# Performance work log

Measured on AMD Instinct MI355X. Metric: run time of the kernel, lower is better.

The kernel has to match this reference:

```python
import jax, jax.numpy as jnp
import numpy as np

EPS = 1e-8  # F.cosine_similarity eps
K = 2       # prompt_length


def setup_inputs() -> dict:
    key = jax.random.key(0)
    k1, k2, k3, k4 = jax.random.split(key, 4)
    B, DIM, NP, D = 32, 64, 4, 1024   # P: [batch, dim, N_p, D]; D == V (rows of stored table)
    E, VC = 768, 32000                 # stored table [V=D, E]; f_e: E -> vocab_dim=VC
    P = jax.random.normal(k1, (B, DIM, NP, D), dtype=jnp.float32)
    we_stored = jax.random.normal(k2, (D, E), dtype=jnp.float32) * 0.02
    fe_w = jax.random.normal(k3, (VC, E), dtype=jnp.float32) * 0.02
    fe_b = jax.random.normal(k4, (VC,), dtype=jnp.float32) * 0.02
    return {"P": P, "we_stored": we_stored, "fe_w": fe_w, "fe_b": fe_b}


def reference(P, we_stored, fe_w, fe_b):
    # word_embeddings = f_e(stored).t()  ->  [vocab_dim, V] == [VC, D]
    T = (we_stored @ fe_w.T + fe_b).T            # [VC, D]
    B, DIM, NP, D = P.shape
    # Cosine sim of each tiled embedding row (repeated N_p times) vs flattened P_i:
    #   dot(tiled_w, P_flat) = w . sum_j P[..., j, :]
    #   ||tiled_w|| = sqrt(N_p) * ||w||
    s = P.sum(axis=2)                                             # [B, DIM, D]
    w_norm = jnp.maximum(jnp.sqrt(jnp.float32(NP)) * jnp.linalg.norm(T, axis=1), EPS)   # [VC]
    p_norm = jnp.maximum(jnp.linalg.norm(P.reshape(B, DIM, -1), axis=-1), EPS)          # [B, DIM]
    scores = jnp.einsum('bdk,vk->bdv', s, T) / (w_norm[None, None, :] * p_norm[..., None])  # [B, DIM, VC]
    values, indices = jax.lax.top_k(scores, K)                    # [B, DIM, K]
    e_k = T[indices]                                              # [B, DIM, K, D]
    Z = jnp.concatenate([e_k, P], axis=2)                         # [B, DIM, NP+K, D]
    return Z, values
```

## Files before the change

kernel.cpp:

```cpp
#include <hip/hip_runtime.h>
#include <hip/hip_bf16.h>
#include <math.h>

#define B_    32
#define DIM_  64
#define NP_   4
#define D_    1024
#define E_    768
#define VC_   32000
#define R_    2048
#define KTOP  2
#define EPS_  1e-8f
#define NCB   250
#define NCAND 8

#define T_OFF    ((size_t)0)
#define S_OFF    (T_OFF + (size_t)VC_ * D_)
#define INVW_OFF (S_OFF + (size_t)R_ * D_)
#define INVP_OFF (INVW_OFF + VC_)
#define WSQ_OFF  (INVP_OFF + R_)
#define PV_OFF   (WSQ_OFF + VC_)
#define PI_OFF   (PV_OFF + (size_t)R_ * NCB * 2)
#define SB_OFF   (PI_OFF + (size_t)R_ * NCB * 2)
#define TB_OFF   (SB_OFF + (size_t)R_ * D_ / 2)
#define WH_OFF   (TB_OFF + (size_t)VC_ * D_ / 2)
#define WL_OFF   (WH_OFF + (size_t)D_ * E_ / 2)
#define CAND_OFF (WL_OFF + (size_t)D_ * E_ / 2)
#define TIDX_OFF (CAND_OFF + (size_t)R_ * NCAND)

#define NEG_INF (-3.4e38f)

typedef __bf16 bf16x8 __attribute__((ext_vector_type(8)));
typedef unsigned short u16x8 __attribute__((ext_vector_type(8)));
typedef float  f32x4  __attribute__((ext_vector_type(4)));

__device__ __forceinline__ unsigned short f2bf(float f) {
    unsigned u = __float_as_uint(f);
    u += 0x7fffu + ((u >> 16) & 1u);
    return (unsigned short)(u >> 16);
}

__device__ __forceinline__ void async_ld16(const void* gptr, void* lptr) {
    __builtin_amdgcn_global_load_lds(
        (const __attribute__((address_space(1))) void*)(uintptr_t)gptr,
        (__attribute__((address_space(3))) void*)(unsigned)(uintptr_t)lptr,
        16, 0, 0);
}

__device__ __forceinline__ bool better(float v, int i, float bv, int bi) {
    return (v > bv) || (v == bv && i < bi);
}

__global__ __launch_bounds__(256) void k_zero(float* __restrict__ wsq) {
    int i = blockIdx.x * 256 + threadIdx.x;
    if (i < VC_) wsq[i] = 0.f;
}

__global__ __launch_bounds__(256) void k_split_we(const float* __restrict__ x,
                                                  unsigned short* __restrict__ hi,
                                                  unsigned short* __restrict__ lo) {
    int i = (blockIdx.x * 256 + threadIdx.x) * 4;
    float4 v = *(const float4*)(x + i);
    ushort4 h, l;
    float e;
    h.x = f2bf(v.x); e = v.x - __uint_as_float((unsigned)h.x << 16); l.x = f2bf(e);
    h.y = f2bf(v.y); e = v.y - __uint_as_float((unsigned)h.y << 16); l.y = f2bf(e);
    h.z = f2bf(v.z); e = v.z - __uint_as_float((unsigned)h.z << 16); l.z = f2bf(e);
    h.w = f2bf(v.w); e = v.w - __uint_as_float((unsigned)h.w << 16); l.w = f2bf(e);
    *(ushort4*)(hi + i) = h;
    *(ushort4*)(lo + i) = l;
}

__global__ __launch_bounds__(256) void k_sum_pnorm(const float* __restrict__ P,
                                                   float* __restrict__ s,
                                                   unsigned short* __restrict__ sb,
                                                   float* __restrict__ invp) {
    int r = blockIdx.x;
    int t = threadIdx.x;
    const float* base = P + (size_t)r * NP_ * D_;
    float4 acc = make_float4(0.f, 0.f, 0.f, 0.f);
    float sq = 0.f;
#pragma unroll
    for (int np = 0; np < NP_; ++np) {
        float4 v = *(const float4*)(base + (size_t)np * D_ + t * 4);
        acc.x += v.x; acc.y += v.y; acc.z += v.z; acc.w += v.w;
        sq += v.x * v.x + v.y * v.y + v.z * v.z + v.w * v.w;
    }
    *(float4*)(s + (size_t)r * D_ + t * 4) = acc;
    ushort4 o;
    o.x = f2bf(acc.x); o.y = f2bf(acc.y); o.z = f2bf(acc.z); o.w = f2bf(acc.w);
    *(ushort4*)(sb + (size_t)r * D_ + t * 4) = o;

    __shared__ float red[256];
    red[t] = sq;
    __syncthreads();
    for (int off = 128; off > 0; off >>= 1) {
        if (t < off) red[t] += red[t + off];
        __syncthreads();
    }
    if (t == 0) invp[r] = 1.0f / fmaxf(sqrtf(red[0]), EPS_);
}

__global__ __launch_bounds__(256) void k_gemm_T_mfma(const float* __restrict__ A,
                                                     const unsigned short* __restrict__ Bh,
                                                     const unsigned short* __restrict__ Bl,
                                                     const float* __restrict__ bias,
                                                     float* __restrict__ T,
                                                     unsigned short* __restrict__ Tb,
                                                     float* __restrict__ wsq) {
    __shared__ __align__(16) float          Af[128 * 32];
    __shared__ __align__(16) unsigned short Bsh[128 * 32];
    __shared__ __align__(16) unsigned short Bsl[128 * 32];

    int tid = threadIdx.x;
    int wid = tid >> 6, lane = tid & 63;
    int quad = lane >> 4, l15 = lane & 15;
    int id  = blockIdx.x;
    int swz = (id & 7) * 250 + (id >> 3);
    int v0 = (swz >> 3) * 128;
    int d0 = (swz & 7) * 128;
    int vband = (wid & 1) * 64, nband = (wid >> 1) * 64;

    f32x4 acc[4][4];
#pragma unroll
    for (int i = 0; i < 4; ++i)
#pragma unroll
        for (int j = 0; j < 4; ++j) acc[i][j] = f32x4{0.f, 0.f, 0.f, 0.f};

    int arow = wid * 32 + (lane >> 3);
    int acol = (lane & 7) * 4;
    int brow = wid * 32 + (lane >> 2);
    int bcol = (lane & 3) * 8;

    for (int k0 = 0; k0 < E_; k0 += 32) {
#pragma unroll
        for (int j = 0; j < 4; ++j)
            async_ld16(A + (size_t)(v0 + arow + j * 8) * E_ + k0 + acol,
                       (void*)(Af + (wid * 32 + j * 8) * 32));
#pragma unroll
        for (int j = 0; j < 2; ++j) {
            async_ld16(Bh + (size_t)(d0 + brow + j * 16) * E_ + k0 + bcol,
                       (void*)(Bsh + (wid * 32 + j * 16) * 32));
            async_ld16(Bl + (size_t)(d0 + brow + j * 16) * E_ + k0 + bcol,
                       (void*)(Bsl + (wid * 32 + j * 16) * 32));
        }
        __syncthreads();

        bf16x8 bh[4], bl[4];
#pragma unroll
        for (int nt = 0; nt < 4; ++nt) {
            bh[nt] = *(const bf16x8*)(Bsh + (nband + nt * 16 + l15) * 32 + quad * 8);
            bl[nt] = *(const bf16x8*)(Bsl + (nband + nt * 16 + l15) * 32 + quad * 8);
        }
#pragma unroll
        for (int mt = 0; mt < 4; ++mt) {
            const float* ap = Af + (vband + mt * 16 + l15) * 32 + quad * 8;
            f32x4 xa = *(const f32x4*)ap;
            f32x4 xb = *(const f32x4*)(ap + 4);
            bf16x8 ah, al;
#pragma unroll
            for (int e = 0; e < 4; ++e) {
                __bf16 h0 = (__bf16)xa[e];
                __bf16 h1 = (__bf16)xb[e];
                ah[e] = h0; ah[e + 4] = h1;
                al[e]     = (__bf16)(xa[e] - (float)h0);
                al[e + 4] = (__bf16)(xb[e] - (float)h1);
            }
#pragma unroll
            for (int nt = 0; nt < 4; ++nt) {
                acc[mt][nt] = __builtin_amdgcn_mfma_f32_16x16x32_bf16(ah, bh[nt], acc[mt][nt], 0, 0, 0);
                acc[mt][nt] = __builtin_amdgcn_mfma_f32_16x16x32_bf16(al, bh[nt], acc[mt][nt], 0, 0, 0);
                acc[mt][nt] = __builtin_amdgcn_mfma_f32_16x16x32_bf16(ah, bl[nt], acc[mt][nt], 0, 0, 0);
            }
        }
        __syncthreads();
    }

    float sq[4][4] = {};
#pragma unroll
    for (int mt = 0; mt < 4; ++mt) {
        int vbase = v0 + vband + mt * 16 + quad * 4;
        float bv[4];
#pragma unroll
        for (int rg = 0; rg < 4; ++rg) bv[rg] = bias[vbase + rg];
#pragma unroll
        for (int nt = 0; nt < 4; ++nt) {
            int d = d0 + nband + nt * 16 + l15;
#pragma unroll
            for (int rg = 0; rg < 4; ++rg) {
                float val = acc[mt][nt][rg] + bv[rg];
                T[(size_t)(vbase + rg) * D_ + d] = val;
                __bf16 vb = (__bf16)val;
                Tb[(size_t)(vbase + rg) * D_ + d] = __builtin_bit_cast(unsigned short, vb);
                sq[mt][rg] += val * val;
            }
        }
    }
#pragma unroll
    for (int mt = 0; mt < 4; ++mt)
#pragma unroll
        for (int rg = 0; rg < 4; ++rg) {
            float p = sq[mt][rg];
            p += __shfl_xor(p, 1); p += __shfl_xor(p, 2);
            p += __shfl_xor(p, 4); p += __shfl_xor(p, 8);
            if (l15 == 0) atomicAdd(&wsq[v0 + vband + mt * 16 + quad * 4 + rg], p);
        }
}

__global__ __launch_bounds__(256) void k_invw(const float* __restrict__ wsq,
                                              float* __restrict__ invw) {
    int v = blockIdx.x * 256 + threadIdx.x;
    if (v < VC_) invw[v] = 1.0f / fmaxf(2.0f * sqrtf(wsq[v]), EPS_);
}

__global__ __launch_bounds__(256) void k_scores_mfma(const unsigned short* __restrict__ Tb,
                                                     const unsigned short* __restrict__ sb,
                                                     const float* __restrict__ invw,
                                                     float* __restrict__ pval,
                                                     int* __restrict__ pidx) {
    __shared__ __align__(16) unsigned short As[2][128 * 32];
    __shared__ __align__(16) unsigned short Bs[2][128 * 32];
    __shared__ float mv[2][128][2];
    __shared__ int   mi[2][128][2];

    int tid = threadIdx.x;
    int wid = tid >> 6, lane = tid & 63;
    int quad = lane >> 4, l15 = lane & 15;
    int id   = blockIdx.x;
    int swz  = (id & 7) * 500 + (id >> 3);
    int vblk = swz >> 4;
    int rblk = swz & 15;
    int v0 = vblk * 128;
    int r0 = rblk * 128;
    int vband = (wid & 1) * 64, rband = (wid >> 1) * 64;

    f32x4 acc[4][4];
#pragma unroll
    for (int i = 0; i < 4; ++i)
#pragma unroll
        for (int j = 0; j < 4; ++j) acc[i][j] = f32x4{0.f, 0.f, 0.f, 0.f};

    int r_lane = lane >> 2;
    int slot   = lane & 3;

#define STAGE_SC(buf, kk)                                                          \
    {                                                                              \
_Pragma("unroll")                                                                  \
        for (int j = 0; j < 2; ++j) {                                              \
            int rowt = wid * 32 + j * 16 + r_lane;                                 \
            int ss = (slot - (rowt >> 1)) & 3;                                     \
            async_ld16(Tb + (size_t)(v0 + rowt) * D_ + (kk) + ss * 8,              \
                       (void*)(As[buf] + (wid * 32 + j * 16) * 32));               \
            async_ld16(sb + (size_t)(r0 + rowt) * D_ + (kk) + ss * 8,              \
                       (void*)(Bs[buf] + (wid * 32 + j * 16) * 32));               \
        }                                                                          \
    }

    int cur = 0;
    STAGE_SC(0, 0);
    __syncthreads();

    for (int k0 = 0; k0 < D_; k0 += 32) {
        if (k0 + 32 < D_) STAGE_SC(cur ^ 1, k0 + 32);

        bf16x8 af[4], bfr[4];
#pragma unroll
        for (int mt = 0; mt < 4; ++mt) {
            int row = vband + mt * 16 + l15;
            int ps = (quad + (row >> 1)) & 3;
            af[mt] = *(const bf16x8*)(As[cur] + row * 32 + ps * 8);
        }
#pragma unroll
        for (int nt = 0; nt < 4; ++nt) {
            int row = rband + nt * 16 + l15;
            int ps = (quad + (row >> 1)) & 3;
            bfr[nt] = *(const bf16x8*)(Bs[cur] + row * 32 + ps * 8);
        }
#pragma unroll
        for (int mt = 0; mt < 4; ++mt)
#pragma unroll
            for (int nt = 0; nt < 4; ++nt)
                acc[mt][nt] = __builtin_amdgcn_mfma_f32_16x16x32_bf16(af[mt], bfr[nt], acc[mt][nt], 0, 0, 0);

        __syncthreads();
        cur ^= 1;
    }

    float iw[4][4];
#pragma unroll
    for (int mt = 0; mt < 4; ++mt)
#pragma unroll
        for (int rg = 0; rg < 4; ++rg)
            iw[mt][rg] = invw[v0 + vband + mt * 16 + quad * 4 + rg];

#pragma unroll
    for (int nt = 0; nt < 4; ++nt) {
        float b1 = NEG_INF, b2 = NEG_INF;
        int i1 = 0x7fffffff, i2 = 0x7fffffff;
#pragma unroll
        for (int mt = 0; mt < 4; ++mt)
#pragma unroll
            for (int rg = 0; rg < 4; ++rg) {
                float val = acc[mt][nt][rg] * iw[mt][rg];
                int v = v0 + vband + mt * 16 + quad * 4 + rg;
                if (better(val, v, b1, i1)) { b2 = b1; i2 = i1; b1 = val; i1 = v; }
                else if (better(val, v, b2, i2)) { b2 = val; i2 = v; }
            }
#pragma unroll
        for (int off = 16; off <= 32; off <<= 1) {
            float o1 = __shfl_xor(b1, off), o2 = __shfl_xor(b2, off);
            int  oi1 = __shfl_xor(i1, off), oi2 = __shfl_xor(i2, off);
            if (better(o1, oi1, b1, i1)) {
                if (better(b1, i1, o2, oi2)) { b2 = b1; i2 = i1; } else { b2 = o2; i2 = oi2; }
                b1 = o1; i1 = oi1;
            } else if (better(o1, oi1, b2, i2)) { b2 = o1; i2 = oi1; }
        }
        if (quad == 0) {
            int rl = rband + nt * 16 + l15;
            mv[wid & 1][rl][0] = b1; mi[wid & 1][rl][0] = i1;
            mv[wid & 1][rl][1] = b2; mi[wid & 1][rl][1] = i2;
        }
    }
    __syncthreads();
    if (tid < 128) {
        float b1 = mv[0][tid][0], b2 = mv[0][tid][1];
        int   i1 = mi[0][tid][0], i2 = mi[0][tid][1];
#pragma unroll
        for (int sl = 0; sl < 2; ++sl) {
            float o = mv[1][tid][sl]; int oi = mi[1][tid][sl];
            if (better(o, oi, b1, i1)) { b2 = b1; i2 = i1; b1 = o; i1 = oi; }
            else if (better(o, oi, b2, i2)) { b2 = o; i2 = oi; }
        }
        size_t off = ((size_t)(r0 + tid) * NCB + vblk) * 2;
        pval[off] = b1;     pidx[off] = i1;
        pval[off + 1] = b2; pidx[off + 1] = i2;
    }
#undef STAGE_SC
}

__global__ __launch_bounds__(256) void k_topk8(const float* __restrict__ pval,
                                               const int* __restrict__ pidx,
                                               int* __restrict__ cands) {
    int r = blockIdx.x, t = threadIdx.x;
    __shared__ float v[512];
    __shared__ int  id[512];
    for (int c = t; c < 512; c += 256) {
        if (c < NCB * 2) { v[c] = pval[(size_t)r * NCB * 2 + c]; id[c] = pidx[(size_t)r * NCB * 2 + c]; }
        else             { v[c] = NEG_INF; id[c] = 0x7fffffff; }
    }
    __syncthreads();
    if (t == 0) {
        float bv[NCAND]; int bi[NCAND];
#pragma unroll
        for (int j = 0; j < NCAND; ++j) { bv[j] = NEG_INF; bi[j] = 0x7fffffff; }
        for (int c = 0; c < NCB * 2; ++c) {
            float x = v[c]; int xi = id[c];
            if (better(x, xi, bv[NCAND - 1], bi[NCAND - 1])) {
                int j = NCAND - 1;
                while (j > 0 && better(x, xi, bv[j - 1], bi[j - 1])) {
                    bv[j] = bv[j - 1]; bi[j] = bi[j - 1]; --j;
                }
                bv[j] = x; bi[j] = xi;
            }
        }
#pragma unroll
        for (int j = 0; j < NCAND; ++j) cands[r * NCAND + j] = bi[j];
    }
}

__global__ __launch_bounds__(256) void k_rescore(const float* __restrict__ s,
                                                 const float* __restrict__ T,
                                                 const int* __restrict__ cands,
                                                 const float* __restrict__ invw,
                                                 const float* __restrict__ invp,
                                                 float* __restrict__ outv,
                                                 int* __restrict__ tidx) {
    int r = blockIdx.x, t = threadIdx.x;
    int cg = t >> 5, l32 = t & 31;
    int c = cands[r * NCAND + cg];
    const float* Trow = T + (size_t)c * D_;
    const float* srow = s + (size_t)r * D_;
    float p = 0.f;
#pragma unroll
    for (int j = 0; j < 8; ++j) {
        int e = (j * 32 + l32) * 4;
        float4 a = *(const float4*)(srow + e);
        float4 b = *(const float4*)(Trow + e);
        p += a.x * b.x + a.y * b.y + a.z * b.z + a.w * b.w;
    }
#pragma unroll
    for (int off = 16; off >= 1; off >>= 1) p += __shfl_xor(p, off);
    __shared__ float sc[NCAND];
    if (l32 == 0) sc[cg] = p;
    __syncthreads();
    if (t == 0) {
        float ip = invp[r];
        float b1 = NEG_INF, b2 = NEG_INF;
        int i1 = 0x7fffffff, i2 = 0x7fffffff;
#pragma unroll
        for (int j = 0; j < NCAND; ++j) {
            int ci = cands[r * NCAND + j];
            float val = sc[j] * invw[ci] * ip;
            if (better(val, ci, b1, i1)) { b2 = b1; i2 = i1; b1 = val; i1 = ci; }
            else if (better(val, ci, b2, i2)) { b2 = val; i2 = ci; }
        }
        outv[(size_t)r * 2 + 0] = b1;
        outv[(size_t)r * 2 + 1] = b2;
        tidx[r * 2 + 0] = i1;
        tidx[r * 2 + 1] = i2;
    }
}

__global__ __launch_bounds__(256) void k_writeZ(const float* __restrict__ P,
                                                const float* __restrict__ T,
                                                const int* __restrict__ tidx,
                                                float* __restrict__ out) {
    int blk = blockIdx.x;
    int r = blk / 6, j = blk - r * 6;
    const float* src;
    if (j < KTOP) src = T + (size_t)tidx[r * 2 + j] * D_;
    else          src = P + ((size_t)r * NP_ + (j - KTOP)) * D_;
    float4 v = *(const float4*)(src + threadIdx.x * 4);
    *(float4*)(out + ((size_t)r * 6 + j) * D_ + threadIdx.x * 4) = v;
}

extern "C" void kernel_launch(void* const* d_in, const int* in_sizes, int n_in,
                              void* d_out, int out_size, void* d_ws, size_t ws_size,
                              hipStream_t stream) {
    const float* P   = (const float*)d_in[0];
    const float* we  = (const float*)d_in[1];
    const float* few = (const float*)d_in[2];
    const float* feb = (const float*)d_in[3];
    float* out = (float*)d_out;
    float* ws  = (float*)d_ws;

    float* T    = ws + T_OFF;
    float* s    = ws + S_OFF;
    float* invw = ws + INVW_OFF;
    float* invp = ws + INVP_OFF;
    float* wsq  = ws + WSQ_OFF;
    float* pval = ws + PV_OFF;
    int*   pidx = (int*)(ws + PI_OFF);
    unsigned short* sb  = (unsigned short*)(ws + SB_OFF);
    unsigned short* Tb  = (unsigned short*)(ws + TB_OFF);
    unsigned short* weh = (unsigned short*)(ws + WH_OFF);
    unsigned short* wel = (unsigned short*)(ws + WL_OFF);
    int*   cands = (int*)(ws + CAND_OFF);
    int*   tidx  = (int*)(ws + TIDX_OFF);
    float* outv = out + (size_t)R_ * 6 * D_;

    k_zero<<<(VC_ + 255) / 256, 256, 0, stream>>>(wsq);
    k_split_we<<<(D_ * E_) / 1024, 256, 0, stream>>>(we, weh, wel);
    k_sum_pnorm<<<R_, 256, 0, stream>>>(P, s, sb, invp);
    k_gemm_T_mfma<<<2000, 256, 0, stream>>>(few, weh, wel, feb, T, Tb, wsq);
    k_invw<<<(VC_ + 255) / 256, 256, 0, stream>>>(wsq, invw);
    k_scores_mfma<<<4000, 256, 0, stream>>>(Tb, sb, invw, pval, pidx);
    k_topk8<<<R_, 256, 0, stream>>>(pval, pidx, cands);
    k_rescore<<<R_, 256, 0, stream>>>(s, T, cands, invw, invp, outv, tidx);
    k_writeZ<<<R_ * 6, 256, 0, stream>>>(P, T, tidx, out);
}
```

Baseline: 683.1 us.

## Pre-split fe_w to bf16 hi/lo and double-buffer T GEMM with swizzled LDS

A separate pass now splits fe_w into bf16 hi/lo arrays once, instead of converting fp32 A tiles inside the GEMM inner loop for every d-block. The T GEMM loads all four operands with async global-to-LDS copies into double buffers, prefetching the next k-slice while the current one is computed. It also rotates 16-byte slots per row to cut LDS bank conflicts. The cost is an extra kernel and about 98MB of extra workspace traffic, plus twice the LDS footprint, which may lower occupancy. The f2bf helper is also replaced by native bf16 casts.

```diff
diff --git a/kernel.cpp b/kernel.cpp
--- a/kernel.cpp
+++ b/kernel.cpp
@@ -27,18 +27,14 @@
 #define WL_OFF   (WH_OFF + (size_t)D_ * E_ / 2)
 #define CAND_OFF (WL_OFF + (size_t)D_ * E_ / 2)
 #define TIDX_OFF (CAND_OFF + (size_t)R_ * NCAND)
+#define AH_OFF   (TIDX_OFF + (size_t)R_ * 2)
+#define AL_OFF   (AH_OFF + (size_t)VC_ * E_ / 2)
 
 #define NEG_INF (-3.4e38f)
 
 typedef __bf16 bf16x8 __attribute__((ext_vector_type(8)));
 typedef unsigned short u16x8 __attribute__((ext_vector_type(8)));
 typedef float  f32x4  __attribute__((ext_vector_type(4)));
-
-__device__ __forceinline__ unsigned short f2bf(float f) {
-    unsigned u = __float_as_uint(f);
-    u += 0x7fffu + ((u >> 16) & 1u);
-    return (unsigned short)(u >> 16);
-}
 
 __device__ __forceinline__ void async_ld16(const void* gptr, void* lptr) {
     __builtin_amdgcn_global_load_lds(
@@ -56,17 +52,17 @@
     if (i < VC_) wsq[i] = 0.f;
 }
 
-__global__ __launch_bounds__(256) void k_split_we(const float* __restrict__ x,
-                                                  unsigned short* __restrict__ hi,
-                                                  unsigned short* __restrict__ lo) {
+__global__ __launch_bounds__(256) void k_split(const float* __restrict__ x,
+                                               unsigned short* __restrict__ hi,
+                                               unsigned short* __restrict__ lo) {
     int i = (blockIdx.x * 256 + threadIdx.x) * 4;
     float4 v = *(const float4*)(x + i);
     ushort4 h, l;
-    float e;
-    h.x = f2bf(v.x); e = v.x - __uint_as_float((unsigned)h.x << 16); l.x = f2bf(e);
-    h.y = f2bf(v.y); e = v.y - __uint_as_float((unsigned)h.y << 16); l.y = f2bf(e);
-    h.z = f2bf(v.z); e = v.z - __uint_as_float((unsigned)h.z << 16); l.z = f2bf(e);
-    h.w = f2bf(v.w); e = v.w - __uint_as_float((unsigned)h.w << 16); l.w = f2bf(e);
+    __bf16 b;
+    b = (__bf16)v.x; h.x = __builtin_bit_cast(unsigned short, b); l.x = __builtin_bit_cast(unsigned short, (__bf16)(v.x - (float)b));
+    b = (__bf16)v.y; h.y = __builtin_bit_cast(unsigned short, b); l.y = __builtin_bit_cast(unsigned short, (__bf16)(v.y - (float)b));
+    b = (__bf16)v.z; h.z = __builtin_bit_cast(unsigned short, b); l.z = __builtin_bit_cast(unsigned short, (__bf16)(v.z - (float)b));
+    b = (__bf16)v.w; h.w = __builtin_bit_cast(unsigned short, b); l.w = __builtin_bit_cast(unsigned short, (__bf16)(v.w - (float)b));
     *(ushort4*)(hi + i) = h;
     *(ushort4*)(lo + i) = l;
 }
@@ -88,7 +84,11 @@
     }
     *(float4*)(s + (size_t)r * D_ + t * 4) = acc;
     ushort4 o;
-    o.x = f2bf(acc.x); o.y = f2bf(acc.y); o.z = f2bf(acc.z); o.w = f2bf(acc.w);
+    __bf16 b;
+    b = (__bf16)acc.x; o.x = __builtin_bit_cast(unsigned short, b);
+    b = (__bf16)acc.y; o.y = __builtin_bit_cast(unsigned short, b);
+    b = (__bf16)acc.z; o.z = __builtin_bit_cast(unsigned short, b);
+    b = (__bf16)acc.w; o.w = __builtin_bit_cast(unsigned short, b);
     *(ushort4*)(sb + (size_t)r * D_ + t * 4) = o;
 
     __shared__ float red[256];
@@ -101,16 +101,18 @@
     if (t == 0) invp[r] = 1.0f / fmaxf(sqrtf(red[0]), EPS_);
 }
 
-__global__ __launch_bounds__(256) void k_gemm_T_mfma(const float* __restrict__ A,
-                                                     const unsigned short* __restrict__ Bh,
-                                                     const unsigned short* __restrict__ Bl,
+__global__ __launch_bounds__(256) void k_gemm_T_mfma(const unsigned short* __restrict__ Ahg,
+                                                     const unsigned short* __restrict__ Alg,
+                                                     const unsigned short* __restrict__ Bhg,
+                                                     const unsigned short* __restrict__ Blg,
                                                      const float* __restrict__ bias,
                                                      float* __restrict__ T,
                                                      unsigned short* __restrict__ Tb,
                                                      float* __restrict__ wsq) {
-    __shared__ __align__(16) float          Af[128 * 32];
-    __shared__ __align__(16) unsigned short Bsh[128 * 32];
-    __shared__ __align__(16) unsigned short Bsl[128 * 32];
+    __shared__ __align__(16) unsigned short Ash[2][128 * 32];
+    __shared__ __align__(16) unsigned short Asl[2][128 * 32];
+    __shared__ __align__(16) unsigned short Bsh[2][128 * 32];
+    __shared__ __align__(16) unsigned short Bsl[2][128 * 32];
 
     int tid = threadIdx.x;
     int wid = tid >> 6, lane = tid & 63;
@@ -127,54 +129,63 @@
 #pragma unroll
         for (int j = 0; j < 4; ++j) acc[i][j] = f32x4{0.f, 0.f, 0.f, 0.f};
 
-    int arow = wid * 32 + (lane >> 3);
-    int acol = (lane & 7) * 4;
-    int brow = wid * 32 + (lane >> 2);
-    int bcol = (lane & 3) * 8;
+    int r_lane = lane >> 2;
+    int slot   = lane & 3;
+
+#define STAGE_G(buf, kk)                                                           \
+    {                                                                              \
+_Pragma("unroll")                                                                  \
+        for (int j = 0; j < 2; ++j) {                                              \
+            int rowt = wid * 32 + j * 16 + r_lane;                                 \
+            int ss = (slot - (rowt >> 1)) & 3;                                     \
+            void* la = (void*)(Ash[buf] + (wid * 32 + j * 16) * 32);               \
+            void* lb = (void*)(Asl[buf] + (wid * 32 + j * 16) * 32);               \
+            void* lc = (void*)(Bsh[buf] + (wid * 32 + j * 16) * 32);               \
+            void* ld = (void*)(Bsl[buf] + (wid * 32 + j * 16) * 32);               \
+            async_ld16(Ahg + (size_t)(v0 + rowt) * E_ + (kk) + ss * 8, la);        \
+            async_ld16(Alg + (size_t)(v0 + rowt) * E_ + (kk) + ss * 8, lb);        \
+            async_ld16(Bhg + (size_t)(d0 + rowt) * E_ + (kk) + ss * 8, lc);        \
+            async_ld16(Blg + (size_t)(d0 + rowt) * E_ + (kk) + ss * 8, ld);        \
+        }                                                                          \
+    }
+
+    int cur = 0;
+    STAGE_G(0, 0);
+    __syncthreads();
 
     for (int k0 = 0; k0 < E_; k0 += 32) {
-#pragma unroll
-        for (int j = 0; j < 4; ++j)
-            async_ld16(A + (size_t)(v0 + arow + j * 8) * E_ + k0 + acol,
-                       (void*)(Af + (wid * 32 + j * 8) * 32));
-#pragma unroll
-        for (int j = 0; j < 2; ++j) {
-            async_ld16(Bh + (size_t)(d0 + brow + j * 16) * E_ + k0 + bcol,
-                       (void*)(Bsh + (wid * 32 + j * 16) * 32));
-            async_ld16(Bl + (size_t)(d0 + brow + j * 16) * E_ + k0 + bcol,
-                       (void*)(Bsl + (wid * 32 + j * 16) * 32));
-        }
+        if (k0 + 32 < E_) STAGE_G(cur ^ 1, k0 + 32);
+
+        bf16x8 fah[4], fal[4], fbh[4], fbl[4];
+#pragma unroll
+        for (int mt = 0; mt < 4; ++mt) {
+            int row = vband + mt * 16 + l15;
+            int ps = (quad + (row >> 1)) & 3;
+            int off = row * 32 + ps * 8;
+            fah[mt] = *(const bf16x8*)(Ash[cur] + off);
+            fal[mt] = *(const bf16x8*)(Asl[cur] + off);
+        }
+#pragma unroll
+        for (int nt = 0; nt < 4; ++nt) {
+            int row = nband + nt * 16 + l15;
+            int ps = (quad + (row >> 1)) & 3;
+            int off = row * 32 + ps * 8;
+            fbh[nt] = *(const bf16x8*)(Bsh[cur] + off);
+            fbl[nt] = *(const bf16x8*)(Bsl[cur] + off);
+        }
+#pragma unroll
+        for (int mt = 0; mt < 4; ++mt)
+#pragma unroll
+            for (int nt = 0; nt < 4; ++nt) {
+                acc[mt][nt] = __builtin_amdgcn_mfma_f32_16x16x32_bf16(fah[mt], fbh[nt], acc[mt][nt], 0, 0, 0);
+                acc[mt][nt] = __builtin_amdgcn_mfma_f32_16x16x32_bf16(fal[mt], fbh[nt], acc[mt][nt], 0, 0, 0);
+                acc[mt][nt] = __builtin_amdgcn_mfma_f32_16x16x32_bf16(fah[mt], fbl[nt], acc[mt][nt], 0, 0, 0);
+            }
+
         __syncthreads();
-
-        bf16x8 bh[4], bl[4];
-#pragma unroll
-        for (int nt = 0; nt < 4; ++nt) {
-            bh[nt] = *(const bf16x8*)(Bsh + (nband + nt * 16 + l15) * 32 + quad * 8);
-            bl[nt] = *(const bf16x8*)(Bsl + (nband + nt * 16 + l15) * 32 + quad * 8);
-        }
-#pragma unroll
-        for (int mt = 0; mt < 4; ++mt) {
-            const float* ap = Af + (vband + mt * 16 + l15) * 32 + quad * 8;
-            f32x4 xa = *(const f32x4*)ap;
-            f32x4 xb = *(const f32x4*)(ap + 4);
-            bf16x8 ah, al;
-#pragma unroll
-            for (int e = 0; e < 4; ++e) {
-                __bf16 h0 = (__bf16)xa[e];
-                __bf16 h1 = (__bf16)xb[e];
-                ah[e] = h0; ah[e + 4] = h1;
-                al[e]     = (__bf16)(xa[e] - (float)h0);
-                al[e + 4] = (__bf16)(xb[e] - (float)h1);
-            }
-#pragma unroll
-            for (int nt = 0; nt < 4; ++nt) {
-                acc[mt][nt] = __builtin_amdgcn_mfma_f32_16x16x32_bf16(ah, bh[nt], acc[mt][nt], 0, 0, 0);
-                acc[mt][nt] = __builtin_amdgcn_mfma_f32_16x16x32_bf16(al, bh[nt], acc[mt][nt], 0, 0, 0);
-                acc[mt][nt] = __builtin_amdgcn_mfma_f32_16x16x32_bf16(ah, bl[nt], acc[mt][nt], 0, 0, 0);
-            }
-        }
-        __syncthreads();
-    }
+        cur ^= 1;
+    }
+#undef STAGE_G
 
     float sq[4][4] = {};
 #pragma unroll
@@ -285,6 +296,7 @@
         __syncthreads();
         cur ^= 1;
     }
+#undef STAGE_SC
 
     float iw[4][4];
 #pragma unroll
@@ -335,7 +347,6 @@
         pval[off] = b1;     pidx[off] = i1;
         pval[off + 1] = b2; pidx[off + 1] = i2;
     }
-#undef STAGE_SC
 }
 
 __global__ __launch_bounds__(256) void k_topk8(const float* __restrict__ pval,
@@ -447,12 +458,15 @@
     unsigned short* wel = (unsigned short*)(ws + WL_OFF);
     int*   cands = (int*)(ws + CAND_OFF);
     int*   tidx  = (int*)(ws + TIDX_OFF);
+    unsigned short* fewh = (unsigned short*)(ws + AH_OFF);
+    unsigned short* fewl = (unsigned short*)(ws + AL_OFF);
     float* outv = out + (size_t)R_ * 6 * D_;
 
     k_zero<<<(VC_ + 255) / 256, 256, 0, stream>>>(wsq);
-    k_split_we<<<(D_ * E_) / 1024, 256, 0, stream>>>(we, weh, wel);
+    k_split<<<(D_ * E_) / 1024, 256, 0, stream>>>(we, weh, wel);
+    k_split<<<((size_t)VC_ * E_) / 1024, 256, 0, stream>>>(few, fewh, fewl);
     k_sum_pnorm<<<R_, 256, 0, stream>>>(P, s, sb, invp);
-    k_gemm_T_mfma<<<2000, 256, 0, stream>>>(few, weh, wel, feb, T, Tb, wsq);
+    k_gemm_T_mfma<<<2000, 256, 0, stream>>>(fewh, fewl, weh, wel, feb, T, Tb, wsq);
     k_invw<<<(VC_ + 255) / 256, 256, 0, stream>>>(wsq, invw);
     k_scores_mfma<<<4000, 256, 0, stream>>>(Tb, sb, invw, pval, pidx);
     k_topk8<<<R_, 256, 0, stream>>>(pval, pidx, cands);
```

Result: no change. 684.6 us (+0.2%).
